# Optimization experiments

Hardware: AMD Instinct MI355X
Metric: run time of the kernel (lower is better)

The kernel has to match this reference:

```python
import jax, jax.numpy as jnp
import numpy as np

DIM = 1024
LN_EPS = 1e-5

def _layernorm(x, w, b):
    m = jnp.mean(x, axis=-1, keepdims=True)
    v = jnp.mean((x - m) ** 2, axis=-1, keepdims=True)
    return (x - m) * jax.lax.rsqrt(v + LN_EPS) * w + b

def _linear(x, w, b):
    # torch Linear: w is (out, in)
    return jnp.einsum('bsd,od->bso', x, w) + b

def setup_inputs() -> dict:
    key = jax.random.key(0)
    ks = jax.random.split(key, 8)
    d = DIM
    s = 0.02
    return {
        'x': jax.random.normal(ks[0], (4, 4096, d), dtype=jnp.float32),
        'ln1_w': jnp.ones((d,), jnp.float32), 'ln1_b': jnp.zeros((d,), jnp.float32),
        'ln2_w': jnp.ones((d,), jnp.float32), 'ln2_b': jnp.zeros((d,), jnp.float32),
        'gate_w': jax.random.normal(ks[1], (d, d), jnp.float32) * s,
        'gate_b': jnp.zeros((d,), jnp.float32),
        'val_w': jax.random.normal(ks[2], (d, d), jnp.float32) * s,
        'val_b': jnp.zeros((d,), jnp.float32),
        'ffn1_w': jax.random.normal(ks[3], (4 * d, d), jnp.float32) * s,
        'ffn1_b': jnp.zeros((4 * d,), jnp.float32),
        'ffn2_w': jax.random.normal(ks[4], (d, 4 * d), jnp.float32) * s,
        'ffn2_b': jnp.zeros((d,), jnp.float32),
    }

def reference(x, ln1_w, ln1_b, ln2_w, ln2_b, gate_w, gate_b, val_w, val_b, ffn1_w, ffn1_b, ffn2_w, ffn2_b):
    batch, seq_len, dim = x.shape
    h = _layernorm(x, ln1_w, ln1_b)
    g = jax.nn.sigmoid(_linear(h, gate_w, gate_b))
    v = _linear(h, val_w, val_b)
    cumsum_v = jnp.cumsum(g * v, axis=1)
    cumsum_g = jnp.cumsum(g, axis=1) + 1e-6
    position = jnp.arange(1, seq_len + 1, dtype=x.dtype)[None, :, None]  # [1,S,1]
    mem = cumsum_v / (jnp.sqrt(cumsum_g) * jnp.sqrt(position / seq_len + 0.1))
    x = x + mem
    h2 = _layernorm(x, ln2_w, ln2_b)
    ff = _linear(jax.nn.gelu(_linear(h2, ffn1_w, ffn1_b), approximate=False), ffn2_w, ffn2_b)
    return x + ff
```

## Files before the change

### kernel.cpp

```cpp
#include <hip/hip_runtime.h>
#include <cstdint>
#include <cstddef>

#define DIMD 1024
#define SEQ  4096
#define BATCH 4
#define MTOT (BATCH*SEQ)
#define NCHUNK 64
#define CLEN   64

typedef __attribute__((ext_vector_type(8))) short short8;
typedef __attribute__((ext_vector_type(4))) float floatx4;

__device__ __forceinline__ unsigned short f2bf(float f){
  unsigned u = __float_as_uint(f);
  u += 0x7fffu + ((u >> 16) & 1u);
  return (unsigned short)(u >> 16);
}
__device__ __forceinline__ float bf2f(unsigned short u){
  return __uint_as_float((unsigned)u << 16);
}

__device__ __forceinline__ void async16(const void* g, void* l){
  __builtin_amdgcn_global_load_lds(
      (const __attribute__((address_space(1))) void*)g,
      (__attribute__((address_space(3))) void*)l, 16, 0, 0);
}

__global__ void f32_to_bf16_kernel(const float* __restrict__ in,
                                   unsigned short* __restrict__ out, int n){
  int i = (blockIdx.x * 256 + threadIdx.x) * 4;
  if (i < n){
    float4 v = *(const float4*)(in + i);
    uint2 o;
    o.x = (unsigned)f2bf(v.x) | ((unsigned)f2bf(v.y) << 16);
    o.y = (unsigned)f2bf(v.z) | ((unsigned)f2bf(v.w) << 16);
    *(uint2*)(out + i) = o;
  }
}

__global__ __launch_bounds__(256)
void ln_kernel(const float* __restrict__ X, const float* __restrict__ w,
               const float* __restrict__ b, unsigned short* __restrict__ H){
  const int row = blockIdx.x;
  const int tid = threadIdx.x;
  const float4 xv = ((const float4*)(X + (size_t)row * DIMD))[tid];
  float s  = xv.x + xv.y + xv.z + xv.w;
  float ss = xv.x*xv.x + xv.y*xv.y + xv.z*xv.z + xv.w*xv.w;
  #pragma unroll
  for (int o = 32; o; o >>= 1){
    s  += __shfl_down(s, o);
    ss += __shfl_down(ss, o);
  }
  __shared__ float ps[4], pss[4], mv[2];
  const int wid = tid >> 6, lane = tid & 63;
  if (lane == 0){ ps[wid] = s; pss[wid] = ss; }
  __syncthreads();
  if (tid == 0){
    float S1 = ps[0]+ps[1]+ps[2]+ps[3];
    float S2 = pss[0]+pss[1]+pss[2]+pss[3];
    float m = S1 * (1.0f / DIMD);
    float var = S2 * (1.0f / DIMD) - m*m;
    mv[0] = m; mv[1] = rsqrtf(var + 1e-5f);
  }
  __syncthreads();
  const float m = mv[0], rs = mv[1];
  const float4 wv = ((const float4*)w)[tid];
  const float4 bv = ((const float4*)b)[tid];
  float o0 = (xv.x - m) * rs * wv.x + bv.x;
  float o1 = (xv.y - m) * rs * wv.y + bv.y;
  float o2 = (xv.z - m) * rs * wv.z + bv.z;
  float o3 = (xv.w - m) * rs * wv.w + bv.w;
  uint2 o;
  o.x = (unsigned)f2bf(o0) | ((unsigned)f2bf(o1) << 16);
  o.y = (unsigned)f2bf(o2) | ((unsigned)f2bf(o3) << 16);
  ((uint2*)(H + (size_t)row * DIMD))[tid] = o;
}

template<int EPI>
__global__ __launch_bounds__(512, 2)
void gemm256(const unsigned short* __restrict__ A, int lda,
             const unsigned short* __restrict__ Bw, int ldb,
             const float* __restrict__ bias, const float* __restrict__ bias2,
             void* __restrict__ OutP, void* __restrict__ Out2P,
             int ldc, int grid_n, int K)
{
  __shared__ char lds[4 * 32768];
  const int tid = threadIdx.x;
  const int bid = ((int)blockIdx.x & 7) * ((int)gridDim.x >> 3) + ((int)blockIdx.x >> 3);
  const int bm = bid / grid_n, bn = bid % grid_n;
  const int row0 = bm * 256, col0 = bn * 256;
  const int wid = tid >> 6, lane = tid & 63;
  const int wr = wid >> 2, wc = wid & 3;
  const int l15 = lane & 15, rq = lane >> 4;

  const int st_sl = (tid & 3) ^ ((tid >> 3) & 3);
  const unsigned short* Asrc = A  + (size_t)(row0 + (tid >> 2)) * lda + st_sl * 8;
  const unsigned short* Bsrc = Bw + (size_t)(col0 + (tid >> 2)) * ldb + st_sl * 8;
  const int st_off = tid * 16;

  floatx4 acc[8][4];
  #pragma unroll
  for (int m = 0; m < 8; ++m)
    #pragma unroll
    for (int n = 0; n < 4; ++n)
      acc[m][n] = (floatx4){0.f, 0.f, 0.f, 0.f};

  auto stage = [&](int buf, int kt){
    const int k0 = kt << 5;
    char* base = lds + buf * 32768;
    #pragma unroll
    for (int i = 0; i < 2; ++i)
      async16(Asrc + (size_t)(i * 128) * lda + k0, base + i * 8192 + st_off);
    #pragma unroll
    for (int i = 0; i < 2; ++i)
      async16(Bsrc + (size_t)(i * 128) * ldb + k0, base + 16384 + i * 8192 + st_off);
  };

  const int nt = K >> 5;
  stage(0, 0); stage(1, 1); stage(2, 2);

  for (int t = 0; t < nt; ++t){
    asm volatile("s_waitcnt vmcnt(8)" ::: "memory");
    asm volatile("s_barrier" ::: "memory");
    const char* La = lds + (t & 3) * 32768;
    const char* Lb = La + 16384;

    auto LD = [&](const char* Lp, int r)->short8 {
      return *(const short8*)(Lp + (r << 6) + ((rq ^ ((r >> 1) & 3)) << 4));
    };
    short8 a0[4], a1[4], bv[4];
    #pragma unroll
    for (int mi = 0; mi < 4; ++mi) a0[mi] = LD(La, wr*128 + mi*16 + l15);
    #pragma unroll
    for (int n = 0; n < 4; ++n)    bv[n]  = LD(Lb, wc*64 + n*16 + l15);
    #pragma unroll
    for (int mi = 0; mi < 4; ++mi) a1[mi] = LD(La, wr*128 + 64 + mi*16 + l15);

    { const int nxt = (t + 3 < nt) ? t + 3 : nt - 1;
      stage((t + 3) & 3, nxt); }

    __builtin_amdgcn_s_setprio(1);
    #pragma unroll
    for (int mi = 0; mi < 4; ++mi)
      #pragma unroll
      for (int n = 0; n < 4; ++n)
        acc[mi][n] = __builtin_amdgcn_mfma_f32_16x16x32_bf16(a0[mi], bv[n], acc[mi][n], 0, 0, 0);
    #pragma unroll
    for (int mi = 0; mi < 4; ++mi)
      #pragma unroll
      for (int n = 0; n < 4; ++n)
        acc[4+mi][n] = __builtin_amdgcn_mfma_f32_16x16x32_bf16(a1[mi], bv[n], acc[4+mi][n], 0, 0, 0);
    __builtin_amdgcn_s_setprio(0);
  }

  if constexpr (EPI == 2 || EPI == 5){
    asm volatile("s_barrier" ::: "memory");
    char* slab = lds + wid * 8192;
    unsigned short* dst; int colw; int ldout; bool sigm = false;
    const float* bsel;
    if constexpr (EPI == 5){
      const int c0 = col0 + wc * 64;
      if (c0 < 1024){ dst = (unsigned short*)OutP;  colw = c0;        bsel = bias;  sigm = true;  }
      else          { dst = (unsigned short*)Out2P; colw = c0 - 1024; bsel = bias2; sigm = false; }
      ldout = 1024;
    } else {
      dst = (unsigned short*)OutP; colw = col0 + wc * 64; bsel = bias; ldout = ldc;
    }
    const int rdrow = lane >> 3;
    const int rdoff = rdrow * 128 + (((lane & 7) ^ (rdrow & 7)) << 4);
    const int rdoff2 = (rdrow + 8) * 128 + (((lane & 7) ^ ((rdrow + 8) & 7)) << 4);
    const int rdsl = (lane & 7) * 16;
    #pragma unroll
    for (int m = 0; m < 8; ++m){
      #pragma unroll
      for (int n = 0; n < 4; ++n){
        const float bs = bsel[colw + n*16 + l15];
        const int cchunk = n*2 + (l15 >> 3);
        #pragma unroll
        for (int j = 0; j < 4; ++j){
          const float val = acc[m][n][j] + bs;
          float r;
          if constexpr (EPI == 2){
            r = 0.5f * val * (1.f + erff(val * 0.70710678118f));
          } else {
            r = sigm ? (1.f / (1.f + expf(-val))) : val;
          }
          const int rr = rq*4 + j;
          *(unsigned short*)(slab + rr*128 + ((cchunk ^ (rr & 7)) << 4) + (l15 & 7)*2) = f2bf(r);
        }
      }
      asm volatile("s_waitcnt lgkmcnt(0)" ::: "memory");
      uint4 w0 = *(const uint4*)(slab + rdoff);
      uint4 w1 = *(const uint4*)(slab + rdoff2);
      asm volatile("s_waitcnt lgkmcnt(0)" ::: "memory");
      const int growb = row0 + wr * 128 + m * 16;
      *(uint4*)((char*)(dst + (size_t)(growb + rdrow) * ldout + colw) + rdsl) = w0;
      *(uint4*)((char*)(dst + (size_t)(growb + rdrow + 8) * ldout + colw) + rdsl) = w1;
    }
  } else {
    #pragma unroll
    for (int n = 0; n < 4; ++n){
      const int col = col0 + wc * 64 + n * 16 + l15;
      const float bs = (EPI == 4) ? 0.f : bias[col];
      #pragma unroll
      for (int m = 0; m < 8; ++m){
        const int rowb = row0 + wr * 128 + m * 16 + rq * 4;
        #pragma unroll
        for (int j = 0; j < 4; ++j){
          const size_t o = (size_t)(rowb + j) * ldc + col;
          float* O = (float*)OutP;
          O[o] = acc[m][n][j] + bs + O[o];
        }
      }
    }
  }
}

__global__ __launch_bounds__(256)
void scan_sums(const unsigned short* __restrict__ G, const unsigned short* __restrict__ V,
               float* __restrict__ SG, float* __restrict__ SGV){
  const int bc = blockIdx.x;
  const int d  = blockIdx.y * 256 + threadIdx.x;
  const int b = bc >> 6, c = bc & 63;
  size_t base = ((size_t)b * SEQ + (size_t)c * CLEN) * DIMD + d;
  float sg = 0.f, sgv = 0.f;
  for (int i = 0; i < CLEN; ++i){
    float g = bf2f(G[base + (size_t)i * DIMD]);
    float v = bf2f(V[base + (size_t)i * DIMD]);
    sg += g; sgv += g * v;
  }
  SG[(size_t)bc * DIMD + d] = sg;
  SGV[(size_t)bc * DIMD + d] = sgv;
}

__global__ __launch_bounds__(256)
void scan_prefix(float* __restrict__ SG, float* __restrict__ SGV){
  const int b = blockIdx.x;
  const int d = blockIdx.y * 256 + threadIdx.x;
  float rg = 0.f, rgv = 0.f;
  for (int c = 0; c < NCHUNK; ++c){
    size_t i = ((size_t)(b * NCHUNK + c)) * DIMD + d;
    float tg = SG[i], tv = SGV[i];
    SG[i] = rg; SGV[i] = rgv;
    rg += tg; rgv += tv;
  }
}

__global__ __launch_bounds__(256)
void scan_final(const unsigned short* __restrict__ G, const unsigned short* __restrict__ V,
                const float* __restrict__ SG, const float* __restrict__ SGV,
                const float* __restrict__ X, float* __restrict__ X2){
  const int bc = blockIdx.x;
  const int d  = blockIdx.y * 256 + threadIdx.x;
  const int b = bc >> 6, c = bc & 63;
  size_t base = ((size_t)b * SEQ + (size_t)c * CLEN) * DIMD + d;
  float rg  = SG[(size_t)bc * DIMD + d];
  float rgv = SGV[(size_t)bc * DIMD + d];
  for (int i = 0; i < CLEN; ++i){
    size_t idx = base + (size_t)i * DIMD;
    float g = bf2f(G[idx]), v = bf2f(V[idx]);
    rg += g; rgv += g * v;
    int s = c * CLEN + i;
    float pf = (float)(s + 1) * (1.0f / SEQ) + 0.1f;
    float mem = rgv * rsqrtf((rg + 1e-6f) * pf);
    X2[idx] = X[idx] + mem;
  }
}

extern "C" void kernel_launch(void* const* d_in, const int* in_sizes, int n_in,
                              void* d_out, int out_size, void* d_ws, size_t ws_size,
                              hipStream_t stream)
{
  const float* x     = (const float*)d_in[0];
  const float* ln1w  = (const float*)d_in[1];
  const float* ln1b  = (const float*)d_in[2];
  const float* ln2w  = (const float*)d_in[3];
  const float* ln2b  = (const float*)d_in[4];
  const float* gatew = (const float*)d_in[5];
  const float* gateb = (const float*)d_in[6];
  const float* valw  = (const float*)d_in[7];
  const float* valb  = (const float*)d_in[8];
  const float* f1w   = (const float*)d_in[9];
  const float* f1b   = (const float*)d_in[10];
  const float* f2w   = (const float*)d_in[11];
  const float* f2b   = (const float*)d_in[12];
  float* out = (float*)d_out;

  const size_t MB = 1024u * 1024u;
  const size_t baseNeed = (size_t)(32+32+32+2+2+8+8)*MB + 2u*BATCH*NCHUNK*DIMD*4 + 4096;
  const bool bigT = (baseNeed + 64u*MB) <= ws_size;

  char* ws = (char*)d_ws;
  size_t off = 0;
  auto alloc = [&](size_t bytes) -> char* {
    char* p = ws + off; off += (bytes + 255) & ~(size_t)255; return p;
  };
  unsigned short* H  = (unsigned short*)alloc((size_t)MTOT * DIMD * 2);
  unsigned short* G  = (unsigned short*)alloc((size_t)MTOT * DIMD * 2);
  unsigned short* V  = (unsigned short*)alloc((size_t)MTOT * DIMD * 2);
  if (bigT) alloc(64u * MB);
  unsigned short* T  = G;
  unsigned short* WGV= (unsigned short*)alloc((size_t)2 * DIMD * DIMD * 2);
  unsigned short* W1 = (unsigned short*)alloc((size_t)4 * DIMD * DIMD * 2);
  unsigned short* W2 = (unsigned short*)alloc((size_t)4 * DIMD * DIMD * 2);
  float* SG  = (float*)alloc((size_t)BATCH * NCHUNK * DIMD * 4);
  float* SGV = (float*)alloc((size_t)BATCH * NCHUNK * DIMD * 4);

  if (off > ws_size) return;

  f32_to_bf16_kernel<<<DIMD*DIMD/1024, 256, 0, stream>>>(gatew, WGV, DIMD*DIMD);
  f32_to_bf16_kernel<<<DIMD*DIMD/1024, 256, 0, stream>>>(valw,  WGV + (size_t)DIMD*DIMD, DIMD*DIMD);
  f32_to_bf16_kernel<<<4*DIMD*DIMD/1024, 256, 0, stream>>>(f1w, W1, 4*DIMD*DIMD);
  f32_to_bf16_kernel<<<4*DIMD*DIMD/1024, 256, 0, stream>>>(f2w, W2, 4*DIMD*DIMD);

  ln_kernel<<<MTOT, 256, 0, stream>>>(x, ln1w, ln1b, H);

  gemm256<5><<<(MTOT/256)*(2048/256), 512, 0, stream>>>(
      H, DIMD, WGV, DIMD, gateb, valb, G, V, 2048, 2048/256, DIMD);

  scan_sums  <<<dim3(BATCH*NCHUNK, DIMD/256), 256, 0, stream>>>(G, V, SG, SGV);
  scan_prefix<<<dim3(BATCH, DIMD/256),        256, 0, stream>>>(SG, SGV);
  scan_final <<<dim3(BATCH*NCHUNK, DIMD/256), 256, 0, stream>>>(G, V, SG, SGV, x, out);

  ln_kernel<<<MTOT, 256, 0, stream>>>(out, ln2w, ln2b, H);

  if (bigT){
    gemm256<2><<<(MTOT/256)*(4096/256), 512, 0, stream>>>(
        H, DIMD, W1, DIMD, f1b, nullptr, T, nullptr, 4*DIMD, 4096/256, DIMD);
    gemm256<3><<<(MTOT/256)*(DIMD/256), 512, 0, stream>>>(
        T, 4*DIMD, W2, 4*DIMD, f2b, nullptr, out, nullptr, DIMD, DIMD/256, 4*DIMD);
  } else {
    for (int c = 0; c < 2; ++c){
      const unsigned short* W1c = W1 + (size_t)c * 2048 * DIMD;
      const unsigned short* W2c = W2 + (size_t)c * 2048;
      gemm256<2><<<(MTOT/256)*(2048/256), 512, 0, stream>>>(
          H, DIMD, W1c, DIMD, f1b + c*2048, nullptr, T, nullptr, 2048, 2048/256, DIMD);
      if (c == 0)
        gemm256<3><<<(MTOT/256)*(DIMD/256), 512, 0, stream>>>(
            T, 2048, W2c, 4*DIMD, f2b, nullptr, out, nullptr, DIMD, DIMD/256, 2048);
      else
        gemm256<4><<<(MTOT/256)*(DIMD/256), 512, 0, stream>>>(
            T, 2048, W2c, 4*DIMD, nullptr, nullptr, out, nullptr, DIMD, DIMD/256, 2048);
    }
  }
}
```

Measured before the change: 553.3 us.

## Restructure GEMM mainloop to a 3-buffer LDS pipeline with precomputed offsets

```diff
diff --git a/kernel.cpp b/kernel.cpp
--- a/kernel.cpp
+++ b/kernel.cpp
@@ -85,7 +85,7 @@
              void* __restrict__ OutP, void* __restrict__ Out2P,
              int ldc, int grid_n, int K)
 {
-  __shared__ char lds[4 * 32768];
+  __shared__ char lds[3 * 32768];
   const int tid = threadIdx.x;
   const int bid = ((int)blockIdx.x & 7) * ((int)gridDim.x >> 3) + ((int)blockIdx.x >> 3);
   const int bm = bid / grid_n, bn = bid % grid_n;
@@ -95,9 +95,17 @@
   const int l15 = lane & 15, rq = lane >> 4;
 
   const int st_sl = (tid & 3) ^ ((tid >> 3) & 3);
-  const unsigned short* Asrc = A  + (size_t)(row0 + (tid >> 2)) * lda + st_sl * 8;
-  const unsigned short* Bsrc = Bw + (size_t)(col0 + (tid >> 2)) * ldb + st_sl * 8;
+  const unsigned short* aP = A  + (size_t)(row0 + (tid >> 2)) * lda + st_sl * 8;
+  const unsigned short* bP = Bw + (size_t)(col0 + (tid >> 2)) * ldb + st_sl * 8;
   const int st_off = tid * 16;
+  const size_t ldaL = (size_t)lda * 128, ldbL = (size_t)ldb * 128;
+
+  const int slp = (rq ^ ((l15 >> 1) & 3)) << 4;
+  int offA[8], offB[4];
+  #pragma unroll
+  for (int m = 0; m < 8; ++m) offA[m] = (wr*128 + m*16 + l15) * 64 + slp;
+  #pragma unroll
+  for (int n = 0; n < 4; ++n) offB[n] = 16384 + (wc*64 + n*16 + l15) * 64 + slp;
 
   floatx4 acc[8][4];
   #pragma unroll
@@ -106,57 +114,51 @@
     for (int n = 0; n < 4; ++n)
       acc[m][n] = (floatx4){0.f, 0.f, 0.f, 0.f};
 
-  auto stage = [&](int buf, int kt){
-    const int k0 = kt << 5;
+  auto stage = [&](int buf, int kel){
     char* base = lds + buf * 32768;
-    #pragma unroll
-    for (int i = 0; i < 2; ++i)
-      async16(Asrc + (size_t)(i * 128) * lda + k0, base + i * 8192 + st_off);
-    #pragma unroll
-    for (int i = 0; i < 2; ++i)
-      async16(Bsrc + (size_t)(i * 128) * ldb + k0, base + 16384 + i * 8192 + st_off);
+    async16(aP + kel,        base + st_off);
+    async16(aP + ldaL + kel, base + 8192  + st_off);
+    async16(bP + kel,        base + 16384 + st_off);
+    async16(bP + ldbL + kel, base + 24576 + st_off);
   };
 
   const int nt = K >> 5;
-  stage(0, 0); stage(1, 1); stage(2, 2);
-
+  stage(0, 0); stage(1, 32);
+  asm volatile("s_waitcnt vmcnt(4)" ::: "memory");
+  asm volatile("s_barrier" ::: "memory");
+
+  int bufi = 0, sbuf = 2, kel = 64;
   for (int t = 0; t < nt; ++t){
-    asm volatile("s_waitcnt vmcnt(8)" ::: "memory");
-    asm volatile("s_barrier" ::: "memory");
-    const char* La = lds + (t & 3) * 32768;
-    const char* Lb = La + 16384;
-
-    auto LD = [&](const char* Lp, int r)->short8 {
-      return *(const short8*)(Lp + (r << 6) + ((rq ^ ((r >> 1) & 3)) << 4));
-    };
-    short8 a0[4], a1[4], bv[4];
-    #pragma unroll
-    for (int mi = 0; mi < 4; ++mi) a0[mi] = LD(La, wr*128 + mi*16 + l15);
-    #pragma unroll
-    for (int n = 0; n < 4; ++n)    bv[n]  = LD(Lb, wc*64 + n*16 + l15);
-    #pragma unroll
-    for (int mi = 0; mi < 4; ++mi) a1[mi] = LD(La, wr*128 + 64 + mi*16 + l15);
-
-    { const int nxt = (t + 3 < nt) ? t + 3 : nt - 1;
-      stage((t + 3) & 3, nxt); }
+    const char* Lp = lds + bufi * 32768;
+    short8 av[8], bv[4];
+    #pragma unroll
+    for (int m = 0; m < 8; ++m) av[m] = *(const short8*)(Lp + offA[m]);
+    #pragma unroll
+    for (int n = 0; n < 4; ++n) bv[n] = *(const short8*)(Lp + offB[n]);
+
+    stage(sbuf, kel);
+    kel += 32;
 
     __builtin_amdgcn_s_setprio(1);
     #pragma unroll
-    for (int mi = 0; mi < 4; ++mi)
+    for (int m = 0; m < 8; ++m)
       #pragma unroll
       for (int n = 0; n < 4; ++n)
-        acc[mi][n] = __builtin_amdgcn_mfma_f32_16x16x32_bf16(a0[mi], bv[n], acc[mi][n], 0, 0, 0);
-    #pragma unroll
-    for (int mi = 0; mi < 4; ++mi)
-      #pragma unroll
-      for (int n = 0; n < 4; ++n)
-        acc[4+mi][n] = __builtin_amdgcn_mfma_f32_16x16x32_bf16(a1[mi], bv[n], acc[4+mi][n], 0, 0, 0);
+        acc[m][n] = __builtin_amdgcn_mfma_f32_16x16x32_bf16(av[m], bv[n], acc[m][n], 0, 0, 0);
     __builtin_amdgcn_s_setprio(0);
-  }
+
+    asm volatile("s_barrier" ::: "memory");
+    asm volatile("s_waitcnt vmcnt(4)" ::: "memory");
+    asm volatile("s_barrier" ::: "memory");
+    if (++bufi == 3) bufi = 0;
+    if (++sbuf == 3) sbuf = 0;
+  }
+
+  asm volatile("s_waitcnt vmcnt(0)" ::: "memory");
+  asm volatile("s_barrier" ::: "memory");
 
   if constexpr (EPI == 2 || EPI == 5){
-    asm volatile("s_barrier" ::: "memory");
-    char* slab = lds + wid * 8192;
+    char* slab = lds + wid * 4096;
     unsigned short* dst; int colw; int ldout; bool sigm = false;
     const float* bsel;
     if constexpr (EPI == 5){
@@ -168,7 +170,7 @@
       dst = (unsigned short*)OutP; colw = col0 + wc * 64; bsel = bias; ldout = ldc;
     }
     const int rdrow = lane >> 3;
-    const int rdoff = rdrow * 128 + (((lane & 7) ^ (rdrow & 7)) << 4);
+    const int rdoff  = rdrow * 128 + (((lane & 7) ^ (rdrow & 7)) << 4);
     const int rdoff2 = (rdrow + 8) * 128 + (((lane & 7) ^ ((rdrow + 8) & 7)) << 4);
     const int rdsl = (lane & 7) * 16;
     #pragma unroll
```

Result: slower. 564.5 us (+2.0%).
